# Kernel tuning notes

Measured on AMD Instinct MI355X. Metric: run time of the kernel, lower is better.

The kernel has to match this reference:

```python
import jax, jax.numpy as jnp
import numpy as np

N_USER = 50000
N_ITEM = 100000
N = N_USER + N_ITEM
NNZ = 3_000_000
EMB = 64
BATCH = 4096


def _l2norm(x, eps=1e-12):
    # torch F.normalize(p=2, dim=1): x / max(||x||, eps)
    n = jnp.sqrt(jnp.sum(x * x, axis=1, keepdims=True))
    return x / jnp.maximum(n, eps)


def setup_inputs() -> dict:
    key = jax.random.key(0)
    ks = jax.random.split(key, 12)
    users = jax.random.randint(ks[0], (BATCH,), 0, N_USER, dtype=jnp.int64 if jax.config.jax_enable_x64 else jnp.int32)
    rows = jax.random.randint(ks[1], (NNZ,), 0, N, dtype=jnp.int32)
    cols = jax.random.randint(ks[2], (NNZ,), 0, N, dtype=jnp.int32)
    vals = jax.random.uniform(ks[3], (NNZ,), dtype=jnp.float32)
    user_emb = jax.random.normal(ks[4], (N_USER, EMB), dtype=jnp.float32) * 0.1
    item_emb = jax.random.normal(ks[5], (N_ITEM, EMB), dtype=jnp.float32) * 0.1
    W0 = jax.random.normal(ks[6], (EMB, EMB), dtype=jnp.float32) * 0.1
    b0 = jax.random.normal(ks[7], (1, EMB), dtype=jnp.float32) * 0.1
    W1 = jax.random.normal(ks[8], (EMB, EMB), dtype=jnp.float32) * 0.1
    b1 = jax.random.normal(ks[9], (1, EMB), dtype=jnp.float32) * 0.1
    W2 = jax.random.normal(ks[10], (EMB, EMB), dtype=jnp.float32) * 0.1
    b2 = jax.random.normal(ks[11], (1, EMB), dtype=jnp.float32) * 0.1
    return {"users": users, "rows": rows, "cols": cols, "vals": vals,
            "user_emb": user_emb, "item_emb": item_emb,
            "W0": W0, "b0": b0, "W1": W1, "b1": b1, "W2": W2, "b2": b2}


def reference(users, rows, cols, vals, user_emb, item_emb, W0, b0, W1, b1, W2, b2):
    ego = jnp.concatenate([user_emb, item_emb], axis=0)  # [N, EMB]
    total = ego  # all_embeddings[0]
    for W, b in ((W0, b0), (W1, b1), (W2, b2)):
        # SpMM: side[r] = sum_e vals[e] * ego[cols[e]] for rows[e]==r
        side = jax.ops.segment_sum(vals[:, None] * ego[cols], rows, num_segments=N)
        ego = jax.nn.leaky_relu(side @ W + b, negative_slope=0.2)
        total = total + _l2norm(ego)
    u_g = total[:N_USER]
    return u_g[users]  # [BATCH, EMB]
```

## Files before the change

kernel.cpp:

```cpp
#include <hip/hip_runtime.h>
#include <hip/hip_fp16.h>

#define N_USER 50000
#define N_ITEM 100000
#define NTOT   150000
#define NNZ    3000000
#define EMB    64
#define BATCH  4096

#define BROWS  128
#define NB     1172
#define BCAP   3008
#define CHUNK  6144
#define NBUCK  489
#define EGO4   (NTOT * EMB / 4)
#define EGOB   2344
#define OUTB   ((BATCH * EMB) / 1024)

typedef unsigned short u16;
typedef unsigned int   u32;
typedef unsigned long long u64;
typedef _Float16 f16;
typedef f16   f16x8 __attribute__((ext_vector_type(8)));
typedef float f32x4 __attribute__((ext_vector_type(4)));

__device__ __forceinline__ void scan_excl(const int* src, int* dst, int* wsum,
                                          int tid, int lane, int w) {
    int carry = 0;
    for (int base = 0; base < NB; base += 1024) {
        int i = base + tid;
        int x = (i < NB) ? src[i] : 0;
        int v = x;
#pragma unroll
        for (int off = 1; off < 64; off <<= 1) {
            int y = __shfl_up(v, off);
            if (lane >= off) v += y;
        }
        if (lane == 63) wsum[w] = v;
        __syncthreads();
        if (tid < 16) {
            int s = wsum[tid];
#pragma unroll
            for (int off = 1; off < 16; off <<= 1) {
                int y = __shfl_up(s, off);
                if (tid >= off) s += y;
            }
            wsum[tid] = s;
        }
        __syncthreads();
        int excl = carry + (w ? wsum[w - 1] : 0) + v - x;
        if (i < NB) dst[i] = excl;
        carry += wsum[15];
        __syncthreads();
    }
}

__global__ __launch_bounds__(1024) void k_prep(const int* __restrict__ rows,
                                               const int* __restrict__ cols,
                                               const float* __restrict__ vals,
                                               int* __restrict__ bcnt,
                                               int2* __restrict__ bbuf,
                                               const float4* __restrict__ ue4,
                                               const float4* __restrict__ ie4,
                                               uint2* __restrict__ ego,
                                               const float* __restrict__ ue,
                                               const int* __restrict__ users,
                                               float* __restrict__ out) {
    int bi = blockIdx.x, tid = threadIdx.x;
    if (bi >= NBUCK) {
        int bj = bi - NBUCK;
        if (bj < EGOB) {
            int i = bj * 1024 + tid;
            if (i < EGO4) {
                const int UF4 = N_USER * EMB / 4;
                float4 f = (i < UF4) ? ue4[i] : ie4[i - UF4];
                __half2 h0 = __floats2half2_rn(f.x, f.y);
                __half2 h1 = __floats2half2_rn(f.z, f.w);
                ego[i] = make_uint2(*(u32*)&h0, *(u32*)&h1);
            }
        } else {
            int t = (bj - EGOB) * 1024 + tid;
            int w = t >> 6, lane = t & 63;
            int u = users[w];
            out[w * EMB + lane] = ue[(size_t)u * EMB + lane];
        }
        return;
    }

    __shared__ int2 stage[CHUNK];
    __shared__ u16  sbuck[CHUNK];
    __shared__ int  hist[NB], cur[NB], gbase[NB];
    __shared__ int  wsum[16];
    int lane = tid & 63, w = tid >> 6;
    int start = bi * CHUNK;
    int n = min(start + CHUNK, NNZ) - start;

    for (int i = tid; i < NB; i += 1024) hist[i] = 0;
    __syncthreads();

    u32 ex[6], ev[6];
    int eb[6];
#pragma unroll
    for (int u = 0; u < 6; ++u) {
        int i = u * 1024 + tid;
        if (i < n) {
            int e = start + i;
            int r = rows[e];
            ex[u] = (u32)cols[e] | ((u32)(r & 127) << 18);
            ev[u] = (u32)__float_as_int(vals[e]);
            eb[u] = r >> 7;
            atomicAdd(&hist[eb[u]], 1);
        }
    }
    __syncthreads();

    for (int i = tid; i < NB; i += 1024) {
        int h = hist[i];
        gbase[i] = h ? atomicAdd(&bcnt[i * 16], h) : 0;
    }
    scan_excl(hist, cur, wsum, tid, lane, w);

#pragma unroll
    for (int u = 0; u < 6; ++u) {
        int i = u * 1024 + tid;
        if (i < n) {
            int pos = atomicAdd(&cur[eb[u]], 1);
            stage[pos] = make_int2((int)ex[u], (int)ev[u]);
            sbuck[pos] = (u16)eb[u];
        }
    }
    __syncthreads();
    for (int j = tid; j < n; j += 1024) {
        int b = sbuck[j];
        int pos = gbase[b] + (j - (cur[b] - hist[b]));
        if (pos < BCAP)
            bbuf[(size_t)b * BCAP + pos] = stage[j];
    }
}

__global__ __launch_bounds__(512) void k_fused(const int* __restrict__ bcnt,
                                               const int2* __restrict__ bbuf,
                                               const f16* __restrict__ ego_in,
                                               const float* __restrict__ W,
                                               const float* __restrict__ bias,
                                               u16* __restrict__ ego_out) {
    __shared__ __align__(16) char ubuf[BCAP * 8];
    __shared__ f16  Wl[64 * 72];
    __shared__ int  hist[128], cur[128], rowptr[129];
    __shared__ int  ws2[2];
    int2* stg = (int2*)ubuf;
    f16*  S16 = (f16*)ubuf;
    int tid = threadIdx.x, lane = tid & 63, w = tid >> 6;

    int b = blockIdx.x;
    int cnt = min(bcnt[b * 16], BCAP);
    const int2* src = bbuf + (size_t)b * BCAP;

    for (int i = tid; i < 4096; i += 512) {
        int k = i >> 6, n = i & 63;
        Wl[n * 72 + k] = (f16)W[i];
    }
    if (tid < 128) hist[tid] = 0;
    __syncthreads();

    u32 fx[6], fv[6];
#pragma unroll
    for (int u = 0; u < 6; ++u) {
        int i = u * 512 + tid;
        if (i < cnt) {
            int2 e = src[i];
            fx[u] = (u32)e.x;
            fv[u] = (u32)e.y;
            atomicAdd(&hist[(fx[u] >> 18) & 127], 1);
        }
    }
    __syncthreads();

    int sx = 0, sv = 0;
    if (tid < 128) {
        sx = hist[tid]; sv = sx;
#pragma unroll
        for (int off = 1; off < 64; off <<= 1) {
            int y = __shfl_up(sv, off);
            if (lane >= off) sv += y;
        }
        if (lane == 63) ws2[tid >> 6] = sv;
    }
    __syncthreads();
    if (tid < 128) {
        int excl = sv - sx + ((tid >= 64) ? ws2[0] : 0);
        rowptr[tid] = excl;
        cur[tid]    = excl;
    }
    if (tid == 0) rowptr[128] = cnt;
    __syncthreads();

#pragma unroll
    for (int u = 0; u < 6; ++u) {
        int i = u * 512 + tid;
        if (i < cnt) {
            int pos = atomicAdd(&cur[(fx[u] >> 18) & 127], 1);
            stg[pos] = make_int2((int)fx[u], (int)fv[u]);
        }
    }
    __syncthreads();

    const char* egob = (const char*)ego_in;
    int slot = lane >> 3, d8 = lane & 7;
    int rA = w * 16 + slot;
    int rB = rA + 8;
    int eA = rowptr[rA], kA = rowptr[rA + 1];
    int eB = rowptr[rB], kB = rowptr[rB + 1];
    float accA[8], accB[8];
#pragma unroll
    for (int j = 0; j < 8; ++j) { accA[j] = 0.f; accB[j] = 0.f; }
    while (__any((eA < kA) || (eB < kB))) {
        bool a0 = eA < kA, a1 = (eA + 1) < kA;
        bool b0 = eB < kB, b1 = (eB + 1) < kB;
        uint4 gA0, gA1, gB0, gB1;
        float vA0 = 0.f, vA1 = 0.f, vB0 = 0.f, vB1 = 0.f;
        if (a0) {
            int2 p = stg[eA];
            gA0 = *(const uint4*)(egob + ((size_t)(p.x & 0x3FFFF) << 7) + d8 * 16);
            vA0 = __int_as_float(p.y);
        }
        if (a1) {
            int2 p = stg[eA + 1];
            gA1 = *(const uint4*)(egob + ((size_t)(p.x & 0x3FFFF) << 7) + d8 * 16);
            vA1 = __int_as_float(p.y);
        }
        if (b0) {
            int2 p = stg[eB];
            gB0 = *(const uint4*)(egob + ((size_t)(p.x & 0x3FFFF) << 7) + d8 * 16);
            vB0 = __int_as_float(p.y);
        }
        if (b1) {
            int2 p = stg[eB + 1];
            gB1 = *(const uint4*)(egob + ((size_t)(p.x & 0x3FFFF) << 7) + d8 * 16);
            vB1 = __int_as_float(p.y);
        }
        if (a0) {
            float2 f0 = __half22float2(*(const __half2*)&gA0.x);
            float2 f1 = __half22float2(*(const __half2*)&gA0.y);
            float2 f2 = __half22float2(*(const __half2*)&gA0.z);
            float2 f3 = __half22float2(*(const __half2*)&gA0.w);
            accA[0] = fmaf(vA0, f0.x, accA[0]); accA[1] = fmaf(vA0, f0.y, accA[1]);
            accA[2] = fmaf(vA0, f1.x, accA[2]); accA[3] = fmaf(vA0, f1.y, accA[3]);
            accA[4] = fmaf(vA0, f2.x, accA[4]); accA[5] = fmaf(vA0, f2.y, accA[5]);
            accA[6] = fmaf(vA0, f3.x, accA[6]); accA[7] = fmaf(vA0, f3.y, accA[7]);
        }
        if (a1) {
            float2 f0 = __half22float2(*(const __half2*)&gA1.x);
            float2 f1 = __half22float2(*(const __half2*)&gA1.y);
            float2 f2 = __half22float2(*(const __half2*)&gA1.z);
            float2 f3 = __half22float2(*(const __half2*)&gA1.w);
            accA[0] = fmaf(vA1, f0.x, accA[0]); accA[1] = fmaf(vA1, f0.y, accA[1]);
            accA[2] = fmaf(vA1, f1.x, accA[2]); accA[3] = fmaf(vA1, f1.y, accA[3]);
            accA[4] = fmaf(vA1, f2.x, accA[4]); accA[5] = fmaf(vA1, f2.y, accA[5]);
            accA[6] = fmaf(vA1, f3.x, accA[6]); accA[7] = fmaf(vA1, f3.y, accA[7]);
        }
        if (b0) {
            float2 f0 = __half22float2(*(const __half2*)&gB0.x);
            float2 f1 = __half22float2(*(const __half2*)&gB0.y);
            float2 f2 = __half22float2(*(const __half2*)&gB0.z);
            float2 f3 = __half22float2(*(const __half2*)&gB0.w);
            accB[0] = fmaf(vB0, f0.x, accB[0]); accB[1] = fmaf(vB0, f0.y, accB[1]);
            accB[2] = fmaf(vB0, f1.x, accB[2]); accB[3] = fmaf(vB0, f1.y, accB[3]);
            accB[4] = fmaf(vB0, f2.x, accB[4]); accB[5] = fmaf(vB0, f2.y, accB[5]);
            accB[6] = fmaf(vB0, f3.x, accB[6]); accB[7] = fmaf(vB0, f3.y, accB[7]);
        }
        if (b1) {
            float2 f0 = __half22float2(*(const __half2*)&gB1.x);
            float2 f1 = __half22float2(*(const __half2*)&gB1.y);
            float2 f2 = __half22float2(*(const __half2*)&gB1.z);
            float2 f3 = __half22float2(*(const __half2*)&gB1.w);
            accB[0] = fmaf(vB1, f0.x, accB[0]); accB[1] = fmaf(vB1, f0.y, accB[1]);
            accB[2] = fmaf(vB1, f1.x, accB[2]); accB[3] = fmaf(vB1, f1.y, accB[3]);
            accB[4] = fmaf(vB1, f2.x, accB[4]); accB[5] = fmaf(vB1, f2.y, accB[5]);
            accB[6] = fmaf(vB1, f3.x, accB[6]); accB[7] = fmaf(vB1, f3.y, accB[7]);
        }
        eA += 2; eB += 2;
    }
    __syncthreads();
    {
        f16x8 hA, hB;
#pragma unroll
        for (int j = 0; j < 8; ++j) { hA[j] = (f16)accA[j]; hB[j] = (f16)accB[j]; }
        *(f16x8*)&S16[rA * 72 + d8 * 8] = hA;
        *(f16x8*)&S16[rB * 72 + d8 * 8] = hB;
    }
    __syncthreads();

    int m = lane & 15, quad = lane >> 4;
    int rowbase = b * BROWS;
    int m0 = w * 16;
    f32x4 C[4] = {{0.f,0.f,0.f,0.f},{0.f,0.f,0.f,0.f},{0.f,0.f,0.f,0.f},{0.f,0.f,0.f,0.f}};
#pragma unroll
    for (int kk = 0; kk < 2; ++kk) {
        f16x8 A = *(const f16x8*)&S16[(m0 + m) * 72 + kk * 32 + quad * 8];
#pragma unroll
        for (int nt = 0; nt < 4; ++nt) {
            f16x8 B = *(const f16x8*)&Wl[(nt * 16 + m) * 72 + kk * 32 + quad * 8];
            C[nt] = __builtin_amdgcn_mfma_f32_16x16x32_f16(A, B, C[nt], 0, 0, 0);
        }
    }
#pragma unroll
    for (int nt = 0; nt < 4; ++nt) {
        float bv = bias[nt * 16 + m];
#pragma unroll
        for (int r = 0; r < 4; ++r) {
            int orow = rowbase + m0 + quad * 4 + r;
            float o = C[nt][r] + bv;
            o = o > 0.f ? o : 0.2f * o;
            if (orow < NTOT) {
                __half hh = __float2half(o);
                ego_out[(size_t)orow * EMB + nt * 16 + m] = *(u16*)&hh;
            }
        }
    }
}

__global__ __launch_bounds__(256) void k_accum(const __half* __restrict__ ego,
                                               const int* __restrict__ users,
                                               float* __restrict__ out) {
    int t = blockIdx.x * 256 + threadIdx.x;
    int w = t >> 6, lane = t & 63;
    int u = users[w];
    float x = __half2float(ego[(size_t)u * EMB + lane]);
    float ss = x * x;
#pragma unroll
    for (int off = 32; off; off >>= 1) ss += __shfl_xor(ss, off);
    float n = sqrtf(ss);
    out[w * EMB + lane] += x / fmaxf(n, 1e-12f);
}

__global__ __launch_bounds__(512) void k_user(const int* __restrict__ bcnt,
                                              const int2* __restrict__ bbuf,
                                              const f16* __restrict__ ego_in,
                                              const float* __restrict__ W,
                                              const float* __restrict__ bias,
                                              const int* __restrict__ users,
                                              float* __restrict__ out) {
    __shared__ float Wl[64 * 64];
    int tid = threadIdx.x, lane = tid & 63, w = tid >> 6;
    for (int i = tid; i < 4096; i += 512) Wl[i] = W[i];
    __syncthreads();

    int wid = blockIdx.x * 8 + w;
    int u = users[wid];
    int b = u >> 7;
    u32 rl = (u32)(u & 127);
    int cnt = min(bcnt[b * 16], BCAP);
    const int2* src = bbuf + (size_t)b * BCAP;

    float acc = 0.f;
    for (int base = 0; base < cnt; base += 64) {
        int j = base + lane;
        int2 e = make_int2(0, 0);
        bool valid = j < cnt;
        if (valid) e = src[j];
        bool m = valid && ((((u32)e.x >> 18) & 127) == rl);
        u64 mask = __ballot(m);
        while (mask) {
            int sl = __ffsll((long long)mask) - 1;
            mask &= mask - 1;
            int col = __shfl(e.x, sl) & 0x3FFFF;
            float v = __int_as_float(__shfl(e.y, sl));
            acc = fmaf(v, (float)ego_in[(size_t)col * EMB + lane], acc);
        }
    }

    float y = bias[lane];
#pragma unroll
    for (int k = 0; k < 64; ++k) {
        float sk = __shfl(acc, k);
        y = fmaf(sk, Wl[k * 64 + lane], y);
    }
    y = y > 0.f ? y : 0.2f * y;
    float ss = y * y;
#pragma unroll
    for (int off = 32; off; off >>= 1) ss += __shfl_xor(ss, off);
    float n = sqrtf(ss);
    out[wid * EMB + lane] += y / fmaxf(n, 1e-12f);
}

extern "C" void kernel_launch(void* const* d_in, const int* in_sizes, int n_in,
                              void* d_out, int out_size, void* d_ws, size_t ws_size,
                              hipStream_t stream) {
    const int*   users = (const int*)d_in[0];
    const int*   rows  = (const int*)d_in[1];
    const int*   cols  = (const int*)d_in[2];
    const float* vals  = (const float*)d_in[3];
    const float* ue    = (const float*)d_in[4];
    const float* ie    = (const float*)d_in[5];
    const float* Ws[3] = {(const float*)d_in[6], (const float*)d_in[8], (const float*)d_in[10]};
    const float* bs[3] = {(const float*)d_in[7], (const float*)d_in[9], (const float*)d_in[11]};
    float* out = (float*)d_out;

    char* p = (char*)d_ws;
    f16*  egoA  = (f16*)p;  p += (size_t)NTOT * EMB * 2;
    f16*  egoB  = (f16*)p;  p += (size_t)NTOT * EMB * 2;
    int2* bbuf  = (int2*)p; p += (size_t)NB * BCAP * 8;
    int*  bcnt  = (int*)p;  p += (size_t)NB * 16 * 4;

    hipMemsetAsync(bcnt, 0, (size_t)NB * 16 * 4, stream);
    k_prep<<<NBUCK + EGOB + OUTB, 1024, 0, stream>>>(
        rows, cols, vals, bcnt, bbuf,
        (const float4*)ue, (const float4*)ie, (uint2*)egoA, ue, users, out);

    f16* bufs[2] = {egoA, egoB};
    for (int l = 0; l < 2; ++l) {
        const f16* src = bufs[l & 1];
        f16*       dst = bufs[(l + 1) & 1];
        k_fused<<<NB, 512, 0, stream>>>(bcnt, bbuf, src, Ws[l], bs[l], (u16*)dst);
        k_accum<<<(BATCH * EMB) / 256, 256, 0, stream>>>((const __half*)dst, users, out);
    }
    k_user<<<BATCH / 8, 512, 0, stream>>>(bcnt, bbuf, (const f16*)egoA,
                                          Ws[2], bs[2], users, out);
}
```

Before: 325.0 us.

## Fuse per-user normalize-accumulate into layer kernel via user linked lists

Builds a per-node linked list of batch positions (head/nxt) in the prep kernel, then has k_fused L2-normalize each output row and accumulate it directly into the batch output for the users that appear in that list. This removes the separate k_accum launches and the re-read of the user rows. It also lowers BCAP, which shrinks shared memory and the bucket buffer and may help occupancy, and it prefetches the next edge chunk in k_user. The memset now covers the head array. Lowering BCAP raises the risk of silently dropping edges from buckets that overflow.

```diff
diff --git a/kernel.cpp b/kernel.cpp
--- a/kernel.cpp
+++ b/kernel.cpp
@@ -10,12 +10,13 @@
 
 #define BROWS  128
 #define NB     1172
-#define BCAP   3008
+#define BCAP   2940
 #define CHUNK  6144
 #define NBUCK  489
 #define EGO4   (NTOT * EMB / 4)
 #define EGOB   2344
 #define OUTB   ((BATCH * EMB) / 1024)
+#define LISTB  4
 
 typedef unsigned short u16;
 typedef unsigned int   u32;
@@ -65,7 +66,9 @@
                                                uint2* __restrict__ ego,
                                                const float* __restrict__ ue,
                                                const int* __restrict__ users,
-                                               float* __restrict__ out) {
+                                               float* __restrict__ out,
+                                               int* __restrict__ head,
+                                               int* __restrict__ nxt) {
     int bi = blockIdx.x, tid = threadIdx.x;
     if (bi >= NBUCK) {
         int bj = bi - NBUCK;
@@ -78,11 +81,17 @@
                 __half2 h1 = __floats2half2_rn(f.z, f.w);
                 ego[i] = make_uint2(*(u32*)&h0, *(u32*)&h1);
             }
-        } else {
+        } else if (bj < EGOB + OUTB) {
             int t = (bj - EGOB) * 1024 + tid;
             int w = t >> 6, lane = t & 63;
             int u = users[w];
             out[w * EMB + lane] = ue[(size_t)u * EMB + lane];
+        } else {
+            int i = (bj - EGOB - OUTB) * 1024 + tid;
+            if (i < BATCH) {
+                int u = users[i];
+                nxt[i] = atomicExch(&head[u], i + 1);
+            }
         }
         return;
     }
@@ -143,7 +152,10 @@
                                                const f16* __restrict__ ego_in,
                                                const float* __restrict__ W,
                                                const float* __restrict__ bias,
-                                               u16* __restrict__ ego_out) {
+                                               u16* __restrict__ ego_out,
+                                               const int* __restrict__ head,
+                                               const int* __restrict__ nxt,
+                                               float* __restrict__ out) {
     __shared__ __align__(16) char ubuf[BCAP * 8];
     __shared__ f16  Wl[64 * 72];
     __shared__ int  hist[128], cur[128], rowptr[129];
@@ -304,34 +316,42 @@
             C[nt] = __builtin_amdgcn_mfma_f32_16x16x32_f16(A, B, C[nt], 0, 0, 0);
         }
     }
-#pragma unroll
-    for (int nt = 0; nt < 4; ++nt) {
-        float bv = bias[nt * 16 + m];
-#pragma unroll
-        for (int r = 0; r < 4; ++r) {
-            int orow = rowbase + m0 + quad * 4 + r;
-            float o = C[nt][r] + bv;
-            o = o > 0.f ? o : 0.2f * o;
-            if (orow < NTOT) {
+    float bv[4];
+#pragma unroll
+    for (int nt = 0; nt < 4; ++nt) bv[nt] = bias[nt * 16 + m];
+#pragma unroll
+    for (int r = 0; r < 4; ++r) {
+        int orow = rowbase + m0 + quad * 4 + r;
+        if (orow < NTOT) {
+            float os[4];
+            float ss = 0.f;
+#pragma unroll
+            for (int nt = 0; nt < 4; ++nt) {
+                float o = C[nt][r] + bv[nt];
+                o = o > 0.f ? o : 0.2f * o;
+                os[nt] = o;
+                ss = fmaf(o, o, ss);
                 __half hh = __float2half(o);
                 ego_out[(size_t)orow * EMB + nt * 16 + m] = *(u16*)&hh;
             }
-        }
-    }
-}
-
-__global__ __launch_bounds__(256) void k_accum(const __half* __restrict__ ego,
-                                               const int* __restrict__ users,
-                                               float* __restrict__ out) {
-    int t = blockIdx.x * 256 + threadIdx.x;
-    int w = t >> 6, lane = t & 63;
-    int u = users[w];
-    float x = __half2float(ego[(size_t)u * EMB + lane]);
-    float ss = x * x;
-#pragma unroll
-    for (int off = 32; off; off >>= 1) ss += __shfl_xor(ss, off);
-    float n = sqrtf(ss);
-    out[w * EMB + lane] += x / fmaxf(n, 1e-12f);
+#pragma unroll
+            for (int off = 1; off < 16; off <<= 1) ss += __shfl_xor(ss, off);
+            if (orow < N_USER) {
+                int h = head[orow];
+                if (h) {
+                    float inv = 1.f / fmaxf(sqrtf(ss), 1e-12f);
+                    do {
+                        int s = h - 1;
+                        float* op = out + (size_t)s * EMB + m;
+#pragma unroll
+                        for (int nt = 0; nt < 4; ++nt)
+                            op[nt * 16] += os[nt] * inv;
+                        h = nxt[s];
+                    } while (h);
+                }
+            }
+        }
+    }
 }
 
 __global__ __launch_bounds__(512) void k_user(const int* __restrict__ bcnt,
@@ -354,12 +374,13 @@
     const int2* src = bbuf + (size_t)b * BCAP;
 
     float acc = 0.f;
+    int2 e = make_int2(0, 0);
+    if (lane < cnt) e = src[lane];
     for (int base = 0; base < cnt; base += 64) {
-        int j = base + lane;
-        int2 e = make_int2(0, 0);
-        bool valid = j < cnt;
-        if (valid) e = src[j];
-        bool m = valid && ((((u32)e.x >> 18) & 127) == rl);
+        int jn = base + 64 + lane;
+        int2 en = make_int2(0, 0);
+        if (jn < cnt) en = src[jn];
+        bool m = (base + lane < cnt) && ((((u32)e.x >> 18) & 127) == rl);
         u64 mask = __ballot(m);
         while (mask) {
             int sl = __ffsll((long long)mask) - 1;
@@ -368,6 +389,7 @@
             float v = __int_as_float(__shfl(e.y, sl));
             acc = fmaf(v, (float)ego_in[(size_t)col * EMB + lane], acc);
         }
+        e = en;
     }
 
     float y = bias[lane];
@@ -402,18 +424,22 @@
     f16*  egoB  = (f16*)p;  p += (size_t)NTOT * EMB * 2;
     int2* bbuf  = (int2*)p; p += (size_t)NB * BCAP * 8;
     int*  bcnt  = (int*)p;  p += (size_t)NB * 16 * 4;
-
-    hipMemsetAsync(bcnt, 0, (size_t)NB * 16 * 4, stream);
-    k_prep<<<NBUCK + EGOB + OUTB, 1024, 0, stream>>>(
+    int*  head  = (int*)p;  p += (size_t)NTOT * 4;
+    int*  nxt   = (int*)p;  p += (size_t)BATCH * 4;
+
+    hipMemsetAsync(bcnt, 0, (size_t)NB * 16 * 4 + (size_t)NTOT * 4, stream);
+
+    k_prep<<<NBUCK + EGOB + OUTB + LISTB, 1024, 0, stream>>>(
         rows, cols, vals, bcnt, bbuf,
-        (const float4*)ue, (const float4*)ie, (uint2*)egoA, ue, users, out);
+        (const float4*)ue, (const float4*)ie, (uint2*)egoA, ue, users, out,
+        head, nxt);
 
     f16* bufs[2] = {egoA, egoB};
     for (int l = 0; l < 2; ++l) {
         const f16* src = bufs[l & 1];
         f16*       dst = bufs[(l + 1) & 1];
-        k_fused<<<NB, 512, 0, stream>>>(bcnt, bbuf, src, Ws[l], bs[l], (u16*)dst);
-        k_accum<<<(BATCH * EMB) / 256, 256, 0, stream>>>((const __half*)dst, users, out);
+        k_fused<<<NB, 512, 0, stream>>>(bcnt, bbuf, src, Ws[l], bs[l],
+                                        (u16*)dst, head, nxt, out);
     }
     k_user<<<BATCH / 8, 512, 0, stream>>>(bcnt, bbuf, (const f16*)egoA,
                                           Ws[2], bs[2], users, out);
```

After: 322.4 us. No clear change (-0.8%).
